# Kernel optimization log

Measured on AMD Instinct MI355X. Metric: run time of the kernel, lower is better.

Reference implementation:

```python
import jax, jax.numpy as jnp
import numpy as np

B, C, H, W = 16, 256, 128, 512
MINW, MINH, AF, HS = 128, 32, 256, 256


def _conv1d(x, w, b, pad):
    # x (B, Cin, L), w (Cout, Cin, K) -> (B, Cout, L)
    y = jax.lax.conv_general_dilated(x, w, (1,), [(pad, pad)],
                                     dimension_numbers=('NCH', 'OIH', 'NCH'))
    return y + b[None, :, None]


def setup_inputs() -> dict:
    key = jax.random.key(0)
    ks = jax.random.split(key, 22)
    def p(i, shape, s=0.05):
        return jax.random.normal(ks[i], shape, jnp.float32) * s
    return dict(
        features=jax.random.normal(ks[0], (B, C, H, W), jnp.float32),
        prev_attn_weights=jax.random.uniform(ks[1], (B, H), jnp.float32),
        coverage_vector=jax.random.uniform(ks[2], (B, H), jnp.float32) * 2.0,
        hidden=jax.random.normal(ks[3], (2, 1, B, HS), jnp.float32),
        dw_w=p(4, (MINW, 1)), dw_b=p(5, (1,)),
        enc_w=p(6, (C, AF)), enc_b=p(7, (AF,)),
        conv_w=p(8, (16, 2, 15)), conv_b=p(9, (16,)),
        dcb_w=p(10, (16, AF)), dcb_b=p(11, (AF,)),
        hid_w=p(12, (HS, AF)), hid_b=p(13, (AF,)),
        align_w=p(14, (AF, 1)), align_b=p(15, (1,)),
        convd_w=p(16, (AF, AF, 5)), convd_b=p(17, (AF,)),
        dh_w=p(18, (MINH, 1)), dh_b=p(19, (1,)),
        dec_w=p(20, (HS + AF, 2)), dec_b=p(21, (2,)),
    )


def reference(features, prev_attn_weights, coverage_vector, hidden,
              dw_w, dw_b, enc_w, enc_b, conv_w, conv_b, dcb_w, dcb_b,
              hid_w, hid_b, align_w, align_b, convd_w, convd_b,
              dh_w, dh_b, dec_w, dec_b):
    b, c, h, w = features.shape
    # AdaptiveMaxPool2d((None, MINW)): W divisible by MINW -> uniform windows
    pooled = features.reshape(b, c, h, MINW, w // MINW).max(-1)   # (B,C,H,MINW)
    h_feat = (pooled @ dw_w + dw_b)[..., 0]                       # (B,C,H)
    s = jnp.einsum('bch,cf->bhf', h_feat, enc_w) + enc_b          # (B,H,AF)
    # location + clamped coverage, InstanceNorm1d (no affine, eps=1e-5)
    cat = jnp.stack([prev_attn_weights,
                     jnp.clip(coverage_vector, 0.0, 1.0)], axis=1)  # (B,2,H)
    mu = cat.mean(-1, keepdims=True)
    var = cat.var(-1, keepdims=True)
    cat = (cat - mu) * jax.lax.rsqrt(var + 1e-5)
    cb = _conv1d(cat, conv_w, conv_b, 7)                          # (B,16,H)
    s = s + jnp.einsum('bkh,kf->bhf', cb, dcb_w) + dcb_b
    hh = hidden[0]                                                # (1,B,HS) = LSTM h
    s = s + (jnp.einsum('lbh,hf->lbf', hh, hid_w) + hid_b).transpose(1, 0, 2)  # (B,1,AF) bcast
    s = jnp.tanh(s)
    align = s @ align_w + align_b                                 # (B,H,1)
    attn = jax.nn.softmax(align, axis=1)[..., 0]                  # (B,H)
    context = jnp.einsum('bchw,bh->bcw', features, attn)          # (B,C,W)
    # learned stop decision
    d = jax.nn.relu(_conv1d(s.transpose(0, 2, 1), convd_w, convd_b, 2))  # (B,AF,H)
    d = d.reshape(b, AF, MINH, h // MINH).max(-1)                 # AdaptiveMaxPool1d(MINH)
    d = jax.nn.relu(d @ dh_w + dh_b)[..., 0]                      # (B,AF)
    d = jnp.concatenate([hh[0], d], axis=1)                       # (B,HS+AF)
    decision = d @ dec_w + dec_b                                  # (B,2)
    return context, attn, decision
```

## Files before the change

kernel.cpp:

```cpp
#include <hip/hip_runtime.h>
#include <hip/hip_bf16.h>
#include <math.h>

#define B_ 16
#define C_ 256
#define H_ 128
#define W_ 512
#define AF_ 256
#define HS_ 256

__global__ void k_pre(const float* __restrict__ convd_w,
                      const float* __restrict__ hidden,
                      const float* __restrict__ hid_w,
                      const float* __restrict__ hid_b,
                      float* __restrict__ w2, float* __restrict__ hv) {
  int bid = blockIdx.x, tid = threadIdx.x;
  if (bid < 256) {
    int f = bid;
#pragma unroll
    for (int q = 0; q < 5; ++q) {
      int r = q * 256 + tid;
      w2[(size_t)r * 256 + f] = convd_w[(size_t)f * 1280 + r];
    }
  } else {
    int b = bid - 256;
    const float* hh = hidden + b * HS_;
    float acc = hid_b[tid];
    for (int k = 0; k < HS_; ++k) acc = fmaf(hh[k], hid_w[k * AF_ + tid], acc);
    hv[b * AF_ + tid] = acc;
  }
}

__global__ void k_pool(const float* __restrict__ feat,
                       const float* __restrict__ dw_w,
                       const float* __restrict__ dw_b,
                       float* __restrict__ hf) {
  int gid = blockIdx.x * blockDim.x + threadIdx.x;
  int wv = gid >> 6;
  int lane = threadIdx.x & 63;
  int base_row = wv * 32;
  float w0 = dw_w[lane], w1 = dw_w[lane + 64], wb = dw_b[0];
  const float4* f4 = reinterpret_cast<const float4*>(feat);
#pragma unroll 4
  for (int r = 0; r < 32; ++r) {
    const float4* row = f4 + (size_t)(base_row + r) * 128;
    float4 a = row[lane];
    float4 b = row[lane + 64];
    float m0 = fmaxf(fmaxf(a.x, a.y), fmaxf(a.z, a.w));
    float m1 = fmaxf(fmaxf(b.x, b.y), fmaxf(b.z, b.w));
    float p = m0 * w0 + m1 * w1;
#pragma unroll
    for (int off = 32; off > 0; off >>= 1) p += __shfl_down(p, off, 64);
    if (lane == 0) hf[base_row + r] = p + wb;
  }
}

__global__ void k_sbuild(const float* __restrict__ pa,
                         const float* __restrict__ cv,
                         const float* __restrict__ hf,
                         const float* __restrict__ enc_w, const float* __restrict__ enc_b,
                         const float* __restrict__ conv_w, const float* __restrict__ conv_b,
                         const float* __restrict__ dcb_w, const float* __restrict__ dcb_b,
                         const float* __restrict__ hv,
                         const float* __restrict__ align_w, const float* __restrict__ align_b,
                         float* __restrict__ sbuf, float* __restrict__ alignv) {
  __shared__ float cat[2][H_];
  __shared__ float stats[4];
  __shared__ float cbl[4][16];
  __shared__ float red[4][4];
  __shared__ float4 hfl[C_];
  int bidx = blockIdx.x;
  int b = bidx >> 5;
  int h0 = (bidx & 31) * 4;
  int tid = threadIdx.x;

  {
    float* hl = reinterpret_cast<float*>(hfl);
#pragma unroll
    for (int q = 0; q < 4; ++q) {
      int t = tid + q * 256;
      int c = t >> 2, j = t & 3;
      hl[t] = hf[(size_t)(b * C_ + c) * H_ + h0 + j];
    }
  }
  if (tid < H_) {
    cat[0][tid] = pa[b * H_ + tid];
    float x = cv[b * H_ + tid];
    cat[1][tid] = fminf(fmaxf(x, 0.f), 1.f);
  }
  __syncthreads();
  if (tid < 2) {
    float s = 0.f, s2 = 0.f;
    for (int t = 0; t < H_; ++t) { float x = cat[tid][t]; s += x; s2 += x * x; }
    float mu = s / (float)H_;
    float var = s2 / (float)H_ - mu * mu;
    stats[tid * 2] = mu;
    stats[tid * 2 + 1] = rsqrtf(var + 1e-5f);
  }
  __syncthreads();
  {
    int ch = tid >> 7, t = tid & 127;
    cat[ch][t] = (cat[ch][t] - stats[ch * 2]) * stats[ch * 2 + 1];
  }
  __syncthreads();
  if (tid < 64) {
    int k = tid & 15, j = tid >> 4;
    int h = h0 + j;
    float acc = conv_b[k];
    for (int c2 = 0; c2 < 2; ++c2)
      for (int t = 0; t < 15; ++t) {
        int hh = h + t - 7;
        if (hh >= 0 && hh < H_) acc += cat[c2][hh] * conv_w[(k * 2 + c2) * 15 + t];
      }
    cbl[j][k] = acc;
  }
  __syncthreads();

  int f = tid;
  float base = enc_b[f] + dcb_b[f] + hv[b * AF_ + f];
  float acc[4];
#pragma unroll
  for (int j = 0; j < 4; ++j) {
    float a = base;
#pragma unroll
    for (int k = 0; k < 16; ++k) a = fmaf(cbl[j][k], dcb_w[k * AF_ + f], a);
    acc[j] = a;
  }
  for (int c = 0; c < C_; ++c) {
    float w = enc_w[c * AF_ + f];
    float4 h4 = hfl[c];
    acc[0] = fmaf(h4.x, w, acc[0]);
    acc[1] = fmaf(h4.y, w, acc[1]);
    acc[2] = fmaf(h4.z, w, acc[2]);
    acc[3] = fmaf(h4.w, w, acc[3]);
  }
  float aw = align_w[f];
  int wvi = tid >> 6, lane = tid & 63;
#pragma unroll
  for (int j = 0; j < 4; ++j) {
    float s = tanhf(acc[j]);
    sbuf[(size_t)(b * H_ + h0 + j) * AF_ + f] = s;
    float v = s * aw;
#pragma unroll
    for (int off = 32; off > 0; off >>= 1) v += __shfl_down(v, off, 64);
    if (lane == 0) red[wvi][j] = v;
  }
  __syncthreads();
  if (tid < 4)
    alignv[b * H_ + h0 + tid] =
        red[0][tid] + red[1][tid] + red[2][tid] + red[3][tid] + align_b[0];
}

__global__ void k_softmax(const float* __restrict__ alignv, float* __restrict__ attn) {
  __shared__ float redm[2], reds[2];
  int b = blockIdx.x, t = threadIdx.x;
  float v = alignv[b * H_ + t];
  float m = v;
#pragma unroll
  for (int off = 32; off > 0; off >>= 1) m = fmaxf(m, __shfl_down(m, off, 64));
  if ((t & 63) == 0) redm[t >> 6] = m;
  __syncthreads();
  float mm = fmaxf(redm[0], redm[1]);
  float e = expf(v - mm);
  float s = e;
#pragma unroll
  for (int off = 32; off > 0; off >>= 1) s += __shfl_down(s, off, 64);
  if ((t & 63) == 0) reds[t >> 6] = s;
  __syncthreads();
  attn[b * H_ + t] = e / (reds[0] + reds[1]);
}

__global__ void k_ctx_dconv(const float* __restrict__ feat, const float* __restrict__ attn,
                            const float* __restrict__ sbuf, const float* __restrict__ w2,
                            const float* __restrict__ convd_b,
                            float* __restrict__ dpool, float* __restrict__ ctx) {
  __shared__ float sw[12][AF_];
  int bidx = blockIdx.x;
  int tid = threadIdx.x;
  if (bidx < 256) {
    int b = bidx >> 4;
    int h0 = (bidx & 15) * 8;
    int f = tid;
    for (int rr = 0; rr < 12; ++rr) {
      int h = h0 - 2 + rr;
      sw[rr][f] = (h >= 0 && h < H_) ? sbuf[(size_t)(b * H_ + h) * AF_ + f] : 0.f;
    }
    __syncthreads();
    float acc[8];
#pragma unroll
    for (int j = 0; j < 8; ++j) acc[j] = 0.f;
    for (int c = 0; c < C_; ++c) {
      float sr[12];
#pragma unroll
      for (int rr = 0; rr < 12; ++rr) sr[rr] = sw[rr][c];
      const float* wp = w2 + (size_t)c * 5 * 256 + f;
#pragma unroll
      for (int t = 0; t < 5; ++t) {
        float wvv = wp[t * 256];
#pragma unroll
        for (int j = 0; j < 8; ++j) acc[j] = fmaf(sr[j + t], wvv, acc[j]);
      }
    }
    float bias = convd_b[f];
#pragma unroll
    for (int j = 0; j < 8; ++j) acc[j] = fmaxf(acc[j] + bias, 0.f);
    float p0 = fmaxf(fmaxf(acc[0], acc[1]), fmaxf(acc[2], acc[3]));
    float p1 = fmaxf(fmaxf(acc[4], acc[5]), fmaxf(acc[6], acc[7]));
    int m0 = (h0 >> 2);
    dpool[(size_t)(b * 32 + m0) * AF_ + f] = p0;
    dpool[(size_t)(b * 32 + m0 + 1) * AF_ + f] = p1;
  } else {
    int cb = bidx - 256;
    int b = cb >> 7;
    int c0 = (cb & 127) * 2;
    float* at = &sw[0][0];
    if (tid < H_) at[tid] = attn[b * H_ + tid];
    __syncthreads();
    int c = c0 + (tid >> 7);
    int wq = tid & 127;
    const float4* f4 = reinterpret_cast<const float4*>(feat) +
                       (size_t)(b * C_ + c) * H_ * (W_ / 4) + wq;
    float4 acc = make_float4(0.f, 0.f, 0.f, 0.f);
#pragma unroll 4
    for (int h = 0; h < H_; ++h) {
      float4 x = f4[(size_t)h * (W_ / 4)];
      float a = at[h];
      acc.x += x.x * a; acc.y += x.y * a; acc.z += x.z * a; acc.w += x.w * a;
    }
    reinterpret_cast<float4*>(ctx)[(size_t)(b * C_ + c) * (W_ / 4) + wq] = acc;
  }
}

__global__ void k_decision(const float* __restrict__ dpool, const float* __restrict__ hidden,
                           const float* __restrict__ dh_w, const float* __restrict__ dh_b,
                           const float* __restrict__ dec_w, const float* __restrict__ dec_b,
                           float* __restrict__ dec_out) {
  __shared__ float ddl[AF_];
  __shared__ float red[4];
  int b = blockIdx.x, tid = threadIdx.x;
  float acc = dh_b[0];
  for (int m = 0; m < 32; ++m) acc = fmaf(dpool[(size_t)(b * 32 + m) * AF_ + tid], dh_w[m], acc);
  ddl[tid] = fmaxf(acc, 0.f);
  __syncthreads();
  int col = tid >> 7, kk = tid & 127;
  float a = 0.f;
#pragma unroll
  for (int q = 0; q < 4; ++q) {
    int idx = kk + 128 * q;
    float x = (idx < 256) ? hidden[b * HS_ + idx] : ddl[idx - 256];
    a = fmaf(x, dec_w[idx * 2 + col], a);
  }
#pragma unroll
  for (int off = 32; off > 0; off >>= 1) a += __shfl_down(a, off, 64);
  if ((tid & 63) == 0) red[tid >> 6] = a;
  __syncthreads();
  if (tid < 2) dec_out[b * 2 + tid] = red[tid * 2] + red[tid * 2 + 1] + dec_b[tid];
}

extern "C" void kernel_launch(void* const* d_in, const int* in_sizes, int n_in,
                              void* d_out, int out_size, void* d_ws, size_t ws_size,
                              hipStream_t stream) {
  const float* feat    = (const float*)d_in[0];
  const float* pa      = (const float*)d_in[1];
  const float* cv      = (const float*)d_in[2];
  const float* hidden  = (const float*)d_in[3];
  const float* dw_w    = (const float*)d_in[4];
  const float* dw_b    = (const float*)d_in[5];
  const float* enc_w   = (const float*)d_in[6];
  const float* enc_b   = (const float*)d_in[7];
  const float* conv_w  = (const float*)d_in[8];
  const float* conv_b  = (const float*)d_in[9];
  const float* dcb_w   = (const float*)d_in[10];
  const float* dcb_b   = (const float*)d_in[11];
  const float* hid_w   = (const float*)d_in[12];
  const float* hid_b   = (const float*)d_in[13];
  const float* align_w = (const float*)d_in[14];
  const float* align_b = (const float*)d_in[15];
  const float* convd_w = (const float*)d_in[16];
  const float* convd_b = (const float*)d_in[17];
  const float* dh_w    = (const float*)d_in[18];
  const float* dh_b    = (const float*)d_in[19];
  const float* dec_w   = (const float*)d_in[20];
  const float* dec_b   = (const float*)d_in[21];

  float* out  = (float*)d_out;
  float* ctx  = out;
  float* attn = out + 2097152;
  float* dec  = out + 2097152 + 2048;

  float* ws     = (float*)d_ws;
  float* hf     = ws;
  float* sbuf   = ws + 524288;
  float* dpool  = ws + 1048576;
  float* hv     = ws + 1179648;
  float* alignv = ws + 1183744;
  float* w2     = ws + 1185792;

  k_pre<<<272, 256, 0, stream>>>(convd_w, hidden, hid_w, hid_b, w2, hv);
  k_pool<<<4096, 256, 0, stream>>>(feat, dw_w, dw_b, hf);
  k_sbuild<<<512, 256, 0, stream>>>(pa, cv, hf, enc_w, enc_b, conv_w, conv_b,
                                    dcb_w, dcb_b, hv, align_w, align_b, sbuf, alignv);
  k_softmax<<<16, 128, 0, stream>>>(alignv, attn);
  k_ctx_dconv<<<2304, 256, 0, stream>>>(feat, attn, sbuf, w2, convd_b, dpool, ctx);
  k_decision<<<16, 256, 0, stream>>>(dpool, hidden, dh_w, dh_b, dec_w, dec_b, dec);
}
```

Baseline: 490.2 us.

## Merge pooling into pre kernel with one row per wave and nontemporal feature loads

Merges the k_pre and k_pool launches into one kernel. Pooling now uses one wave per row across 131072 extra blocks, instead of 32 rows per wave, and reads features with nontemporal loads. The context pass also uses nontemporal loads and stores and walks its blocks in reverse order, probably to reuse feature data still in cache from the pooling pass. k_sbuild drops its shared-memory staging of hf and reads it directly from global memory. The trade-offs are a very large grid with little work per wave and uncoalesced scalar hf reads in k_sbuild.

```diff
diff --git a/kernel.cpp b/kernel.cpp
--- a/kernel.cpp
+++ b/kernel.cpp
@@ -9,11 +9,17 @@
 #define AF_ 256
 #define HS_ 256
 
-__global__ void k_pre(const float* __restrict__ convd_w,
-                      const float* __restrict__ hidden,
-                      const float* __restrict__ hid_w,
-                      const float* __restrict__ hid_b,
-                      float* __restrict__ w2, float* __restrict__ hv) {
+typedef float f4v __attribute__((ext_vector_type(4)));
+
+__global__ void k_pre_pool(const float* __restrict__ feat,
+                           const float* __restrict__ dw_w,
+                           const float* __restrict__ dw_b,
+                           const float* __restrict__ convd_w,
+                           const float* __restrict__ hidden,
+                           const float* __restrict__ hid_w,
+                           const float* __restrict__ hid_b,
+                           float* __restrict__ hf, float* __restrict__ w2,
+                           float* __restrict__ hv) {
   int bid = blockIdx.x, tid = threadIdx.x;
   if (bid < 256) {
     int f = bid;
@@ -22,36 +28,24 @@
       int r = q * 256 + tid;
       w2[(size_t)r * 256 + f] = convd_w[(size_t)f * 1280 + r];
     }
-  } else {
+  } else if (bid < 272) {
     int b = bid - 256;
     const float* hh = hidden + b * HS_;
     float acc = hid_b[tid];
     for (int k = 0; k < HS_; ++k) acc = fmaf(hh[k], hid_w[k * AF_ + tid], acc);
     hv[b * AF_ + tid] = acc;
-  }
-}
-
-__global__ void k_pool(const float* __restrict__ feat,
-                       const float* __restrict__ dw_w,
-                       const float* __restrict__ dw_b,
-                       float* __restrict__ hf) {
-  int gid = blockIdx.x * blockDim.x + threadIdx.x;
-  int wv = gid >> 6;
-  int lane = threadIdx.x & 63;
-  int base_row = wv * 32;
-  float w0 = dw_w[lane], w1 = dw_w[lane + 64], wb = dw_b[0];
-  const float4* f4 = reinterpret_cast<const float4*>(feat);
-#pragma unroll 4
-  for (int r = 0; r < 32; ++r) {
-    const float4* row = f4 + (size_t)(base_row + r) * 128;
-    float4 a = row[lane];
-    float4 b = row[lane + 64];
+  } else {
+    int wid = (bid - 272) * 4 + (tid >> 6);
+    int lane = tid & 63;
+    const f4v* row = reinterpret_cast<const f4v*>(feat) + (size_t)wid * 128;
+    f4v a = __builtin_nontemporal_load(row + lane);
+    f4v b = __builtin_nontemporal_load(row + lane + 64);
     float m0 = fmaxf(fmaxf(a.x, a.y), fmaxf(a.z, a.w));
     float m1 = fmaxf(fmaxf(b.x, b.y), fmaxf(b.z, b.w));
-    float p = m0 * w0 + m1 * w1;
+    float p = m0 * dw_w[lane] + m1 * dw_w[lane + 64];
 #pragma unroll
     for (int off = 32; off > 0; off >>= 1) p += __shfl_down(p, off, 64);
-    if (lane == 0) hf[base_row + r] = p + wb;
+    if (lane == 0) hf[wid] = p + dw_b[0];
   }
 }
 
@@ -68,21 +62,11 @@
   __shared__ float stats[4];
   __shared__ float cbl[4][16];
   __shared__ float red[4][4];
-  __shared__ float4 hfl[C_];
   int bidx = blockIdx.x;
   int b = bidx >> 5;
   int h0 = (bidx & 31) * 4;
   int tid = threadIdx.x;
 
-  {
-    float* hl = reinterpret_cast<float*>(hfl);
-#pragma unroll
-    for (int q = 0; q < 4; ++q) {
-      int t = tid + q * 256;
-      int c = t >> 2, j = t & 3;
-      hl[t] = hf[(size_t)(b * C_ + c) * H_ + h0 + j];
-    }
-  }
   if (tid < H_) {
     cat[0][tid] = pa[b * H_ + tid];
     float x = cv[b * H_ + tid];
@@ -126,13 +110,11 @@
     for (int k = 0; k < 16; ++k) a = fmaf(cbl[j][k], dcb_w[k * AF_ + f], a);
     acc[j] = a;
   }
+  const float* hfb = hf + (size_t)(b * C_) * H_ + h0;
   for (int c = 0; c < C_; ++c) {
     float w = enc_w[c * AF_ + f];
-    float4 h4 = hfl[c];
-    acc[0] = fmaf(h4.x, w, acc[0]);
-    acc[1] = fmaf(h4.y, w, acc[1]);
-    acc[2] = fmaf(h4.z, w, acc[2]);
-    acc[3] = fmaf(h4.w, w, acc[3]);
+#pragma unroll
+    for (int j = 0; j < 4; ++j) acc[j] = fmaf(hfb[c * H_ + j], w, acc[j]);
   }
   float aw = align_w[f];
   int wvi = tid >> 6, lane = tid & 63;
@@ -206,11 +188,11 @@
     for (int j = 0; j < 8; ++j) acc[j] = fmaxf(acc[j] + bias, 0.f);
     float p0 = fmaxf(fmaxf(acc[0], acc[1]), fmaxf(acc[2], acc[3]));
     float p1 = fmaxf(fmaxf(acc[4], acc[5]), fmaxf(acc[6], acc[7]));
-    int m0 = (h0 >> 2);
+    int m0 = h0 >> 2;
     dpool[(size_t)(b * 32 + m0) * AF_ + f] = p0;
     dpool[(size_t)(b * 32 + m0 + 1) * AF_ + f] = p1;
   } else {
-    int cb = bidx - 256;
+    int cb = 2303 - bidx;
     int b = cb >> 7;
     int c0 = (cb & 127) * 2;
     float* at = &sw[0][0];
@@ -218,16 +200,17 @@
     __syncthreads();
     int c = c0 + (tid >> 7);
     int wq = tid & 127;
-    const float4* f4 = reinterpret_cast<const float4*>(feat) +
-                       (size_t)(b * C_ + c) * H_ * (W_ / 4) + wq;
-    float4 acc = make_float4(0.f, 0.f, 0.f, 0.f);
+    const f4v* f4 = reinterpret_cast<const f4v*>(feat) +
+                    (size_t)(b * C_ + c) * H_ * (W_ / 4) + wq;
+    f4v acc = (f4v){0.f, 0.f, 0.f, 0.f};
 #pragma unroll 4
     for (int h = 0; h < H_; ++h) {
-      float4 x = f4[(size_t)h * (W_ / 4)];
+      f4v x = __builtin_nontemporal_load(f4 + (size_t)h * (W_ / 4));
       float a = at[h];
       acc.x += x.x * a; acc.y += x.y * a; acc.z += x.z * a; acc.w += x.w * a;
     }
-    reinterpret_cast<float4*>(ctx)[(size_t)(b * C_ + c) * (W_ / 4) + wq] = acc;
+    __builtin_nontemporal_store(acc,
+        reinterpret_cast<f4v*>(ctx) + (size_t)(b * C_ + c) * (W_ / 4) + wq);
   }
 }
 
@@ -291,13 +274,13 @@
   float* ws     = (float*)d_ws;
   float* hf     = ws;
   float* sbuf   = ws + 524288;
-  float* dpool  = ws + 1048576;
-  float* hv     = ws + 1179648;
-  float* alignv = ws + 1183744;
-  float* w2     = ws + 1185792;
-
-  k_pre<<<272, 256, 0, stream>>>(convd_w, hidden, hid_w, hid_b, w2, hv);
-  k_pool<<<4096, 256, 0, stream>>>(feat, dw_w, dw_b, hf);
+  float* hv     = ws + 1048576;
+  float* alignv = ws + 1052672;
+  float* w2     = ws + 1054720;
+  float* dpool  = ws + 1382400;
+
+  k_pre_pool<<<131344, 256, 0, stream>>>(feat, dw_w, dw_b, convd_w, hidden,
+                                         hid_w, hid_b, hf, w2, hv);
   k_sbuild<<<512, 256, 0, stream>>>(pa, cv, hf, enc_w, enc_b, conv_w, conv_b,
                                     dcb_w, dcb_b, hv, align_w, align_b, sbuf, alignv);
   k_softmax<<<16, 128, 0, stream>>>(alignv, attn);
```

Measured after the change: 396.7 us (median of 2 runs). 1.24x faster.
